# Kernel optimization log

Hardware: AMD Instinct MI355X
Metric: run time of the kernel (lower is better)

Reference implementation:

```python
import jax, jax.numpy as jnp
import numpy as np

D, NH, DH, DM = 1024, 16, 64, 4096
B, S = 2, 2048
EPS = 1e-5


def _layernorm(x, w, b):
    mu = jnp.mean(x, axis=-1, keepdims=True)
    var = jnp.mean((x - mu) ** 2, axis=-1, keepdims=True)
    return (x - mu) * jax.lax.rsqrt(var + EPS) * w + b


def setup_inputs() -> dict:
    key = jax.random.key(0)
    ks = jax.random.split(key, 8)
    scale = D ** (-0.5)
    x = jax.random.normal(ks[0], (B, S, D), dtype=jnp.float32)
    WQ = jax.random.normal(ks[1], (NH, D, DH), dtype=jnp.float32) * scale
    WK = jax.random.normal(ks[2], (NH, D, DH), dtype=jnp.float32) * scale
    WV = jax.random.normal(ks[3], (NH, D, DH), dtype=jnp.float32) * scale
    WO = jax.random.normal(ks[4], (NH, DH, D), dtype=jnp.float32) * scale
    # MLP: torch Linear default init ~ U(-1/sqrt(fan_in), 1/sqrt(fan_in)); stored as [in, out]
    W1 = jax.random.uniform(ks[5], (D, DM), dtype=jnp.float32, minval=-1.0, maxval=1.0) * D ** (-0.5)
    b1 = jnp.zeros((DM,), dtype=jnp.float32)
    W2 = jax.random.uniform(ks[6], (DM, D), dtype=jnp.float32, minval=-1.0, maxval=1.0) * DM ** (-0.5)
    b2 = jnp.zeros((D,), dtype=jnp.float32)
    ln1_w = jnp.ones((D,), dtype=jnp.float32)
    ln1_b = jnp.zeros((D,), dtype=jnp.float32)
    ln2_w = jnp.ones((D,), dtype=jnp.float32)
    ln2_b = jnp.zeros((D,), dtype=jnp.float32)
    return {"x": x, "WQ": WQ, "WK": WK, "WV": WV, "WO": WO,
            "W1": W1, "b1": b1, "W2": W2, "b2": b2,
            "ln1_w": ln1_w, "ln1_b": ln1_b, "ln2_w": ln2_w, "ln2_b": ln2_b}


def reference(x, WQ, WK, WV, WO, W1, b1, W2, b2, ln1_w, ln1_b, ln2_w, ln2_b):
    s = x.shape[1]
    dh = WQ.shape[-1]
    r = x
    h = _layernorm(x, ln1_w, ln1_b)
    # batched across all heads (original loops over h; math identical)
    Q = jnp.einsum('bsd,hde->bhse', h, WQ)
    K = jnp.einsum('bsd,hde->bhse', h, WK)
    V = jnp.einsum('bsd,hde->bhse', h, WV)
    scores = jnp.einsum('bhqe,bhke->bhqk', Q, K) / jnp.sqrt(jnp.float32(dh))
    causal = jnp.tril(jnp.ones((s, s), dtype=bool))  # True = keep
    scores = jnp.where(causal, scores, -jnp.inf)
    attn = jax.nn.softmax(scores, axis=-1)
    ctx = jnp.einsum('bhqk,bhke->bhqe', attn, V)
    ao = jnp.einsum('bhqe,hed->bqd', ctx, WO)  # sum over heads
    x = r + ao
    h2 = _layernorm(x, ln2_w, ln2_b)
    mlp = jax.nn.gelu(h2 @ W1 + b1, approximate=False) @ W2 + b2
    return x + mlp
```

## Files before the change

kernel.cpp:

```cpp
#include <hip/hip_runtime.h>
#include <hip/hip_bf16.h>
#include <cstdint>

#define D_MODEL 1024
#define NHEADS 16
#define DHEAD 64
#define DMLP 4096
#define BATCH 2
#define SEQ 2048
#define ROWS (BATCH*SEQ)
#define LN_EPS 1e-5f

typedef __attribute__((ext_vector_type(8))) short short8;
typedef __attribute__((ext_vector_type(4))) float f32x4;

typedef const __attribute__((address_space(1))) uint32_t* gas_ptr;
typedef __attribute__((address_space(3))) uint32_t* las_ptr;

__device__ __forceinline__ short f2bf(float f) {
  union { float f; uint32_t u; } v; v.f = f;
  uint32_t r = v.u + 0x7FFFu + ((v.u >> 16) & 1u);
  return (short)(r >> 16);
}
__device__ __forceinline__ float bf2f(short s) {
  union { uint32_t u; float f; } v; v.u = ((uint32_t)(uint16_t)s) << 16;
  return v.f;
}

__global__ void ln_kernel(const float* __restrict__ x, const float* __restrict__ w,
                          const float* __restrict__ b, short* __restrict__ out) {
  int row = blockIdx.x;
  int t = threadIdx.x;
  const float4 v = ((const float4*)(x + (size_t)row * D_MODEL))[t];
  float s = v.x + v.y + v.z + v.w;
  float s2 = v.x*v.x + v.y*v.y + v.z*v.z + v.w*v.w;
#pragma unroll
  for (int k = 1; k < 64; k <<= 1) { s += __shfl_xor(s, k); s2 += __shfl_xor(s2, k); }
  __shared__ float red[8];
  int wv = t >> 6;
  if ((t & 63) == 0) { red[wv] = s; red[wv + 4] = s2; }
  __syncthreads();
  s = red[0] + red[1] + red[2] + red[3];
  s2 = red[4] + red[5] + red[6] + red[7];
  float mu = s * (1.0f / D_MODEL);
  float var = s2 * (1.0f / D_MODEL) - mu * mu;
  float rstd = rsqrtf(var + LN_EPS);
  const float4 wv4 = ((const float4*)w)[t];
  const float4 bv4 = ((const float4*)b)[t];
  short4 o4;
  o4.x = f2bf((v.x - mu) * rstd * wv4.x + bv4.x);
  o4.y = f2bf((v.y - mu) * rstd * wv4.y + bv4.y);
  o4.z = f2bf((v.z - mu) * rstd * wv4.z + bv4.z);
  o4.w = f2bf((v.w - mu) * rstd * wv4.w + bv4.w);
  *(short4*)(out + (size_t)row * D_MODEL + t * 4) = o4;
}

__global__ void reduce_ln(float* __restrict__ out, const float* __restrict__ part,
                          const float* __restrict__ w, const float* __restrict__ b,
                          short* __restrict__ h2) {
  int row = blockIdx.x;
  int t = threadIdx.x;
  float4 v = ((float4*)(out + (size_t)row * D_MODEL))[t];
  const float4 q = ((const float4*)(part + (size_t)row * D_MODEL))[t];
  v.x += q.x; v.y += q.y; v.z += q.z; v.w += q.w;
  ((float4*)(out + (size_t)row * D_MODEL))[t] = v;
  float s = v.x + v.y + v.z + v.w;
  float s2 = v.x*v.x + v.y*v.y + v.z*v.z + v.w*v.w;
#pragma unroll
  for (int k = 1; k < 64; k <<= 1) { s += __shfl_xor(s, k); s2 += __shfl_xor(s2, k); }
  __shared__ float red[8];
  int wv = t >> 6;
  if ((t & 63) == 0) { red[wv] = s; red[wv + 4] = s2; }
  __syncthreads();
  s = red[0] + red[1] + red[2] + red[3];
  s2 = red[4] + red[5] + red[6] + red[7];
  float mu = s * (1.0f / D_MODEL);
  float var = s2 * (1.0f / D_MODEL) - mu * mu;
  float rstd = rsqrtf(var + LN_EPS);
  const float4 wv4 = ((const float4*)w)[t];
  const float4 bv4 = ((const float4*)b)[t];
  short4 o4;
  o4.x = f2bf((v.x - mu) * rstd * wv4.x + bv4.x);
  o4.y = f2bf((v.y - mu) * rstd * wv4.y + bv4.y);
  o4.z = f2bf((v.z - mu) * rstd * wv4.z + bv4.z);
  o4.w = f2bf((v.w - mu) * rstd * wv4.w + bv4.w);
  *(short4*)(h2 + (size_t)row * D_MODEL + t * 4) = o4;
}

__global__ __launch_bounds__(256) void repack_w(const float* __restrict__ W, short* __restrict__ out,
                                                int nkt, int ks1, int ks2, int ns1, int ns2) {
  const int cp = blockIdx.x, kt = blockIdx.y;
  const int t = threadIdx.x;
  const int cc = t & 127;
  const int kh = t >> 7;
  const int n = cp * 128 + cc;
  const int nbase = (n >> 6) * ns1 + (n & 63) * ns2;
  short* dst = out + (((size_t)cp * nkt + kt) * 128 + cc) * 64;
#pragma unroll
  for (int ci = 0; ci < 4; ci++) {
    const int c = kh * 4 + ci;
    short8 ch;
#pragma unroll
    for (int j = 0; j < 8; j++) {
      int k = kt * 64 + c * 8 + j;
      ch[j] = f2bf(W[(k >> 6) * ks1 + (k & 63) * ks2 + nbase]);
    }
    const int sp = c ^ (cc & 7);
    *(short8*)(dst + sp * 8) = ch;
  }
}

template<int EPI>
__global__ __launch_bounds__(256) void gemm_bt(const short* __restrict__ A, const short* __restrict__ Bpk,
    const float* __restrict__ bias, const float* __restrict__ resid,
    float* __restrict__ outf, short* __restrict__ outb, float* __restrict__ part,
    int M, int N, int K, int LDA, int KFULL) {
  __shared__ alignas(16) short As[2][8192];
  __shared__ alignas(16) short Bs[2][8192];
  const int t = threadIdx.x;
  const int l = t & 63, w = t >> 6;
  const int l15 = l & 15, l4 = l >> 4;

  const int nx = gridDim.x;
  const int sw = nx >> 3;
  int dd = blockIdx.y * nx + blockIdx.x;
  const int xcd = dd & 7, li = dd >> 3;
  const int bx = xcd * sw + (li % sw);
  const int by = li / sw;
  const int row0 = by * 128, col0 = bx * 128;

  const int NKT = KFULL >> 6;
  int ktB = 0;
  if (EPI == 5) {
    A  += (size_t)blockIdx.z * K;
    ktB = blockIdx.z * (K >> 6);
  }
  const short* Bpan = Bpk + (size_t)bx * NKT * 8192;

  f32x4 acc[4][4] = {};

  char* AsB = (char*)As;
  char* BsB = (char*)Bs;

  auto stg = [&](int ti) {
    const int bo = (ti & 1) * 16384;
    const int k0 = ti << 6;
    const short* bsrc = Bpan + (size_t)(ktB + ti) * 8192;
#pragma unroll
    for (int i = 0; i < 4; i++) {
      const int g = i * 256 + t;
      const int gr = g >> 3, sp = g & 7;
      const int co = k0 + ((sp ^ (gr & 7)) << 3);
      __builtin_amdgcn_global_load_lds((gas_ptr)(A + (size_t)(row0 + gr) * LDA + co),
                                       (las_ptr)(AsB + bo + g * 16), 16, 0, 0);
      __builtin_amdgcn_global_load_lds((gas_ptr)(bsrc + (size_t)g * 8),
                                       (las_ptr)(BsB + bo + g * 16), 16, 0, 0);
    }
  };

  const int nk = K >> 6;
  stg(0);
  asm volatile("s_waitcnt vmcnt(0)" ::: "memory");
  __builtin_amdgcn_s_barrier();

  const int wr = (w >> 1) * 64, wc = (w & 1) * 64;

  for (int ti = 0; ti < nk; ti++) {
    const int bo = (ti & 1) * 16384;
    if (ti + 1 < nk) stg(ti + 1);
#pragma unroll
    for (int kg = 0; kg < 2; kg++) {
      const int sl = ((kg * 4 + l4) ^ (l15 & 7)) * 16;
      short8 a[4], bfr[4];
#pragma unroll
      for (int m = 0; m < 4; m++) a[m]   = *(const short8*)(AsB + bo + (wr + m * 16 + l15) * 128 + sl);
#pragma unroll
      for (int n = 0; n < 4; n++) bfr[n] = *(const short8*)(BsB + bo + (wc + n * 16 + l15) * 128 + sl);
#pragma unroll
      for (int m = 0; m < 4; m++)
#pragma unroll
        for (int n = 0; n < 4; n++)
          acc[m][n] = __builtin_amdgcn_mfma_f32_16x16x32_bf16(a[m], bfr[n], acc[m][n], 0, 0, 0);
    }
    if (ti + 1 < nk) { asm volatile("s_waitcnt vmcnt(0)" ::: "memory"); }
    __builtin_amdgcn_s_barrier();
  }

#pragma unroll
  for (int m = 0; m < 4; m++) {
#pragma unroll
    for (int n = 0; n < 4; n++) {
#pragma unroll
      for (int j = 0; j < 4; j++) {
        int R_ = row0 + wr + m * 16 + l4 * 4 + j;
        int C_ = col0 + wc + n * 16 + l15;
        float v = acc[m][n][j];
        size_t o = (size_t)R_ * N + C_;
        if (EPI == 0) {
          outb[o] = f2bf(v);
        } else if (EPI == 2) {
          float xx = v + bias[C_];
          outb[o] = f2bf(0.5f * xx * (1.0f + erff(xx * 0.70710678118f)));
        } else if (EPI == 5) {
          if (blockIdx.z == 0) outf[o] = v + (bias ? bias[C_] : 0.0f) + resid[o];
          else part[o] = v;
        }
      }
    }
  }
}

__global__ void reduce1(float* __restrict__ out, const float* __restrict__ p, int n4) {
  for (int i = blockIdx.x * 256 + threadIdx.x; i < n4; i += gridDim.x * 256) {
    float4 o = ((float4*)out)[i];
    float4 q = ((const float4*)p)[i];
    o.x += q.x; o.y += q.y; o.z += q.z; o.w += q.w;
    ((float4*)out)[i] = o;
  }
}

__device__ __forceinline__ void attn_step(
    int kt_, int qt, int bufP,
    const short* __restrict__ base, const short* __restrict__ vbase,
    short8& vWA, short8& vWB,
    short8& vLA, short8& vLB,
    const short8 qf[2],
    char* KsB, char* VtB, char* PlB,
    f32x4 acc[4], float mrun[4], float lrun[4],
    int w, int l, int q0, int vr, int vd0)
{
  const int l15 = l & 15, l4 = l >> 4;
  const int bufQ = bufP ^ 1;
  if (kt_ < qt) {
#pragma unroll
    for (int i = 0; i < 8; i++) {
      int d = vd0 + i;
      int cs = (vr >> 2) ^ ((d >> 3) & 7);
      uint32_t val = (uint32_t)(uint16_t)vWA[i] | ((uint32_t)(uint16_t)vWB[i] << 16);
      *(uint32_t*)(VtB + bufQ * 9216 + d * 144 + cs * 16 + (vr & 3) * 4) = val;
    }
#pragma unroll
    for (int i = 0; i < 2; i++) {
      int g = (w * 2 + i) * 64 + l;
      int key = g >> 3, ck = g & 7;
      const short* src = base + (size_t)((kt_ + 1) * 64 + key) * 3072 + 1024 + ((ck ^ (key & 7)) * 8);
      __builtin_amdgcn_global_load_lds((gas_ptr)src, (las_ptr)(KsB + bufQ * 8192 + g * 16), 16, 0, 0);
    }
  }
  if (kt_ + 2 <= qt) {
    vLA = *(const short8*)(vbase + (size_t)((kt_ + 2) * 64 + 2 * vr) * 3072);
    vLB = *(const short8*)(vbase + (size_t)((kt_ + 2) * 64 + 2 * vr + 1) * 3072);
  }

  f32x4 sc[4];
#pragma unroll
  for (int cb = 0; cb < 4; cb++) {
    f32x4 s = {};
    int key = cb * 16 + l15;
#pragma unroll
    for (int c = 0; c < 2; c++) {
      int ck = (c * 4 + l4) ^ (key & 7);
      short8 kf = *(const short8*)(KsB + bufP * 8192 + key * 128 + ck * 16);
      s = __builtin_amdgcn_mfma_f32_16x16x32_bf16(qf[c], kf, s, 0, 0, 0);
    }
    sc[cb] = s;
  }

  const bool lastt = (kt_ == qt);
  float alpha[4];
#pragma unroll
  for (int jj = 0; jj < 4; jj++) {
    int qg = q0 + l4 * 4 + jj;
    float s0 = sc[0][jj] * 0.125f;
    float s1 = sc[1][jj] * 0.125f;
    float s2 = sc[2][jj] * 0.125f;
    float s3 = sc[3][jj] * 0.125f;
    if (lastt) {
      int kg = kt_ * 64 + l15;
      if (kg      > qg) s0 = -1e30f;
      if (kg + 16 > qg) s1 = -1e30f;
      if (kg + 32 > qg) s2 = -1e30f;
      if (kg + 48 > qg) s3 = -1e30f;
    }
    float rm = fmaxf(fmaxf(s0, s1), fmaxf(s2, s3));
    rm = fmaxf(rm, __shfl_xor(rm, 1));
    rm = fmaxf(rm, __shfl_xor(rm, 2));
    rm = fmaxf(rm, __shfl_xor(rm, 4));
    rm = fmaxf(rm, __shfl_xor(rm, 8));
    float nm = fmaxf(mrun[jj], rm);
    float al = __expf(mrun[jj] - nm);
    mrun[jj] = nm;
    float p0 = __expf(s0 - nm), p1 = __expf(s1 - nm);
    float p2 = __expf(s2 - nm), p3 = __expf(s3 - nm);
    float ps = p0 + p1 + p2 + p3;
    ps += __shfl_xor(ps, 1);
    ps += __shfl_xor(ps, 2);
    ps += __shfl_xor(ps, 4);
    ps += __shfl_xor(ps, 8);
    lrun[jj] = lrun[jj] * al + ps;
    alpha[jj] = al;
    short* pr = (short*)(PlB + (l4 * 4 + jj) * 144);
    pr[l15]      = f2bf(p0);
    pr[16 + l15] = f2bf(p1);
    pr[32 + l15] = f2bf(p2);
    pr[48 + l15] = f2bf(p3);
  }
#pragma unroll
  for (int db = 0; db < 4; db++) {
    f32x4 a = acc[db];
    a[0] *= alpha[0]; a[1] *= alpha[1]; a[2] *= alpha[2]; a[3] *= alpha[3];
    acc[db] = a;
  }
#pragma unroll
  for (int kc = 0; kc < 2; kc++) {
    short8 pf = *(const short8*)(PlB + l15 * 144 + kc * 64 + l4 * 16);
#pragma unroll
    for (int db = 0; db < 4; db++) {
      int d = db * 16 + l15;
      int cs = (kc * 4 + l4) ^ ((d >> 3) & 7);
      short8 vf = *(const short8*)(VtB + bufP * 9216 + d * 144 + cs * 16);
      acc[db] = __builtin_amdgcn_mfma_f32_16x16x32_bf16(pf, vf, acc[db], 0, 0, 0);
    }
  }
}

__global__ __launch_bounds__(256) void attn_mfma(const short* __restrict__ qkv, short* __restrict__ ctx) {
  __shared__ alignas(16) short Ks[2 * 64 * 64];
  __shared__ alignas(16) short Vt[2 * 64 * 72];
  __shared__ alignas(16) short Pl[4][16 * 72];
  const int t = threadIdx.x;
  const int l = t & 63;
  const int w = t >> 6;
  const int l15 = l & 15, l4 = l >> 4;
  const int bh = blockIdx.x;
  const int b = bh >> 4, h = bh & 15;
  const int qt = (gridDim.y - 1) - blockIdx.y;
  const int q0 = qt * 64 + w * 16;

  const short* base = qkv + (size_t)b * SEQ * 3072 + h * 64;

  short8 qf[2];
#pragma unroll
  for (int c = 0; c < 2; c++)
    qf[c] = *(const short8*)(base + (size_t)(q0 + l15) * 3072 + c * 32 + l4 * 8);

  const int vr = t >> 3;
  const int vd0 = (t & 7) * 8;
  const short* vbase = base + 2048 + vd0;

  char* KsB = (char*)Ks;
  char* VtB = (char*)Vt;
  char* PlB = (char*)&Pl[w][0];

  short8 va0, vb0, va1, vb1;
  va0 = *(const short8*)(vbase + (size_t)(2 * vr) * 3072);
  vb0 = *(const short8*)(vbase + (size_t)(2 * vr + 1) * 3072);
  if (qt >= 1) {
    va1 = *(const short8*)(vbase + (size_t)(64 + 2 * vr) * 3072);
    vb1 = *(const short8*)(vbase + (size_t)(64 + 2 * vr + 1) * 3072);
  }
#pragma unroll
  for (int i = 0; i < 8; i++) {
    int d = vd0 + i;
    int cs = (vr >> 2) ^ ((d >> 3) & 7);
    uint32_t val = (uint32_t)(uint16_t)va0[i] | ((uint32_t)(uint16_t)vb0[i] << 16);
    *(uint32_t*)(VtB + d * 144 + cs * 16 + (vr & 3) * 4) = val;
  }
#pragma unroll
  for (int i = 0; i < 2; i++) {
    int g = (w * 2 + i) * 64 + l;
    int key = g >> 3, ck = g & 7;
    const short* src = base + (size_t)key * 3072 + 1024 + ((ck ^ (key & 7)) * 8);
    __builtin_amdgcn_global_load_lds((gas_ptr)src, (las_ptr)(KsB + g * 16), 16, 0, 0);
  }
  __syncthreads();

  f32x4 acc[4] = {};
  float mrun[4] = {-1e30f, -1e30f, -1e30f, -1e30f};
  float lrun[4] = {0.f, 0.f, 0.f, 0.f};

  int kt = 0;
  while (true) {
    attn_step(kt, qt, 0, base, vbase, va1, vb1, va0, vb0, qf,
              KsB, VtB, PlB, acc, mrun, lrun, w, l, q0, vr, vd0);
    __syncthreads();
    if (++kt > qt) break;
    attn_step(kt, qt, 1, base, vbase, va0, vb0, va1, vb1, qf,
              KsB, VtB, PlB, acc, mrun, lrun, w, l, q0, vr, vd0);
    __syncthreads();
    if (++kt > qt) break;
  }

  float inv[4];
#pragma unroll
  for (int jj = 0; jj < 4; jj++) inv[jj] = 1.0f / lrun[jj];
  short* obase = ctx + (size_t)(b * SEQ + q0) * D_MODEL + h * 64;
#pragma unroll
  for (int db = 0; db < 4; db++)
#pragma unroll
    for (int jj = 0; jj < 4; jj++)
      obase[(size_t)(l4 * 4 + jj) * D_MODEL + db * 16 + l15] = f2bf(acc[db][jj] * inv[jj]);
}

extern "C" void kernel_launch(void* const* d_in, const int* in_sizes, int n_in,
                              void* d_out, int out_size, void* d_ws, size_t ws_size,
                              hipStream_t stream) {
  (void)in_sizes; (void)n_in; (void)out_size; (void)ws_size;
  const float* x    = (const float*)d_in[0];
  const float* WQ   = (const float*)d_in[1];
  const float* WK   = (const float*)d_in[2];
  const float* WV   = (const float*)d_in[3];
  const float* WO   = (const float*)d_in[4];
  const float* W1   = (const float*)d_in[5];
  const float* b1   = (const float*)d_in[6];
  const float* W2   = (const float*)d_in[7];
  const float* b2   = (const float*)d_in[8];
  const float* ln1w = (const float*)d_in[9];
  const float* ln1b = (const float*)d_in[10];
  const float* ln2w = (const float*)d_in[11];
  const float* ln2b = (const float*)d_in[12];
  float* out = (float*)d_out;

  char* p = (char*)d_ws;
  short* h1    = (short*)p; p += (size_t)ROWS * D_MODEL * 2;
  short* ctx   = (short*)p; p += (size_t)ROWS * D_MODEL * 2;
  short* h2    = (short*)p; p += (size_t)ROWS * D_MODEL * 2;
  short* m1    = (short*)p; p += (size_t)ROWS * DMLP * 2;
  short* wqkvT = (short*)p; p += (size_t)3 * D_MODEL * D_MODEL * 2;
  short* woT   = (short*)p; p += (size_t)D_MODEL * D_MODEL * 2;
  short* w1T   = (short*)p; p += (size_t)D_MODEL * DMLP * 2;
  short* w2T   = (short*)p; p += (size_t)D_MODEL * DMLP * 2;
  short* qkv   = (short*)p; p += (size_t)ROWS * 3 * D_MODEL * 2;

  float* fp1 = (float*)qkv;

  repack_w<<<dim3(8, 16), 256, 0, stream>>>(WQ, wqkvT,                 16, 4096, 64, 65536, 1);
  repack_w<<<dim3(8, 16), 256, 0, stream>>>(WK, wqkvT + 8 * 16 * 8192, 16, 4096, 64, 65536, 1);
  repack_w<<<dim3(8, 16), 256, 0, stream>>>(WV, wqkvT + 16 * 16 * 8192, 16, 4096, 64, 65536, 1);
  repack_w<<<dim3(8, 16), 256, 0, stream>>>(WO, woT, 16, 65536, 1024, 64, 1);
  repack_w<<<dim3(32, 16), 256, 0, stream>>>(W1, w1T, 16, 262144, 4096, 64, 1);
  repack_w<<<dim3(8, 64), 256, 0, stream>>>(W2, w2T, 64, 65536, 1024, 64, 1);

  ln_kernel<<<ROWS, 256, 0, stream>>>(x, ln1w, ln1b, h1);
  gemm_bt<0><<<dim3(3 * D_MODEL / 128, ROWS / 128), 256, 0, stream>>>(
      h1, wqkvT, nullptr, nullptr, nullptr, qkv, nullptr,
      ROWS, 3 * D_MODEL, D_MODEL, D_MODEL, D_MODEL);
  attn_mfma<<<dim3(BATCH * NHEADS, SEQ / 64), 256, 0, stream>>>(qkv, ctx);
  gemm_bt<5><<<dim3(D_MODEL / 128, ROWS / 128, 2), 256, 0, stream>>>(
      ctx, woT, nullptr, x, out, nullptr, fp1,
      ROWS, D_MODEL, D_MODEL / 2, D_MODEL, D_MODEL);
  reduce_ln<<<ROWS, 256, 0, stream>>>(out, fp1, ln2w, ln2b, h2);
  gemm_bt<2><<<dim3(DMLP / 128, ROWS / 128), 256, 0, stream>>>(
      h2, w1T, b1, nullptr, nullptr, m1, nullptr,
      ROWS, DMLP, D_MODEL, D_MODEL, D_MODEL);
  gemm_bt<5><<<dim3(D_MODEL / 128, ROWS / 128, 2), 256, 0, stream>>>(
      m1, w2T, b2, out, out, nullptr, fp1,
      ROWS, D_MODEL, DMLP / 2, DMLP, DMLP);
  reduce1<<<2048, 256, 0, stream>>>(out, fp1, ROWS * D_MODEL / 4);
}
```

Baseline: 299.9 us.

## Double attention query tile per block and precompute GEMM staging pointers

The attention kernel now gives each block 128 queries, with each wave handling 32 rows, so every K/V tile loaded into LDS is reused by twice as many queries. The grid halves and uses an interleaved long/short tile order for load balance. Causal masking is applied whenever a key tile overlaps the wave's query range. The GEMM staging loop also precomputes its global and LDS addresses and advances them incrementally instead of recomputing swizzled offsets each tile. The cost is higher register pressure and fewer blocks for the attention kernel.

```diff
diff --git a/kernel.cpp b/kernel.cpp
--- a/kernel.cpp
+++ b/kernel.cpp
@@ -135,31 +135,36 @@
     A  += (size_t)blockIdx.z * K;
     ktB = blockIdx.z * (K >> 6);
   }
-  const short* Bpan = Bpk + (size_t)bx * NKT * 8192;
 
   f32x4 acc[4][4] = {};
-
   char* AsB = (char*)As;
   char* BsB = (char*)Bs;
 
-  auto stg = [&](int ti) {
-    const int bo = (ti & 1) * 16384;
-    const int k0 = ti << 6;
-    const short* bsrc = Bpan + (size_t)(ktB + ti) * 8192;
+  const short* aP[4];
+#pragma unroll
+  for (int i = 0; i < 4; i++) {
+    const int g = i * 256 + t;
+    const int gr = g >> 3, sp = g & 7;
+    aP[i] = A + (size_t)(row0 + gr) * LDA + ((sp ^ (gr & 7)) << 3);
+  }
+  const short* bP = Bpk + ((size_t)bx * NKT + ktB) * 8192 + t * 8;
+  const int d16 = t * 16;
+  int sb = 0;
+
+  auto stg = [&]() {
 #pragma unroll
     for (int i = 0; i < 4; i++) {
-      const int g = i * 256 + t;
-      const int gr = g >> 3, sp = g & 7;
-      const int co = k0 + ((sp ^ (gr & 7)) << 3);
-      __builtin_amdgcn_global_load_lds((gas_ptr)(A + (size_t)(row0 + gr) * LDA + co),
-                                       (las_ptr)(AsB + bo + g * 16), 16, 0, 0);
-      __builtin_amdgcn_global_load_lds((gas_ptr)(bsrc + (size_t)g * 8),
-                                       (las_ptr)(BsB + bo + g * 16), 16, 0, 0);
-    }
+      __builtin_amdgcn_global_load_lds((gas_ptr)(aP[i]),          (las_ptr)(AsB + sb + i * 4096 + d16), 16, 0, 0);
+      __builtin_amdgcn_global_load_lds((gas_ptr)(bP + i * 2048),  (las_ptr)(BsB + sb + i * 4096 + d16), 16, 0, 0);
+    }
+#pragma unroll
+    for (int i = 0; i < 4; i++) aP[i] += 64;
+    bP += 8192;
+    sb ^= 16384;
   };
 
   const int nk = K >> 6;
-  stg(0);
+  stg();
   asm volatile("s_waitcnt vmcnt(0)" ::: "memory");
   __builtin_amdgcn_s_barrier();
 
@@ -167,7 +172,7 @@
 
   for (int ti = 0; ti < nk; ti++) {
     const int bo = (ti & 1) * 16384;
-    if (ti + 1 < nk) stg(ti + 1);
+    if (ti + 1 < nk) stg();
 #pragma unroll
     for (int kg = 0; kg < 2; kg++) {
       const int sl = ((kg * 4 + l4) ^ (l15 & 7)) * 16;
@@ -220,18 +225,18 @@
 }
 
 __device__ __forceinline__ void attn_step(
-    int kt_, int qt, int bufP,
+    int kt_, int ntm1, int bufP,
     const short* __restrict__ base, const short* __restrict__ vbase,
     short8& vWA, short8& vWB,
     short8& vLA, short8& vLB,
-    const short8 qf[2],
+    const short8 qf[2][2],
     char* KsB, char* VtB, char* PlB,
-    f32x4 acc[4], float mrun[4], float lrun[4],
-    int w, int l, int q0, int vr, int vd0)
+    f32x4 acc[2][4], float mrun[2][4], float lrun[2][4],
+    int w, int l, int q0w, int vr, int vd0)
 {
   const int l15 = l & 15, l4 = l >> 4;
   const int bufQ = bufP ^ 1;
-  if (kt_ < qt) {
+  if (kt_ < ntm1) {
 #pragma unroll
     for (int i = 0; i < 8; i++) {
       int d = vd0 + i;
@@ -247,79 +252,87 @@
       __builtin_amdgcn_global_load_lds((gas_ptr)src, (las_ptr)(KsB + bufQ * 8192 + g * 16), 16, 0, 0);
     }
   }
-  if (kt_ + 2 <= qt) {
+  if (kt_ + 2 <= ntm1) {
     vLA = *(const short8*)(vbase + (size_t)((kt_ + 2) * 64 + 2 * vr) * 3072);
     vLB = *(const short8*)(vbase + (size_t)((kt_ + 2) * 64 + 2 * vr + 1) * 3072);
   }
 
-  f32x4 sc[4];
+  f32x4 sc[2][4];
 #pragma unroll
   for (int cb = 0; cb < 4; cb++) {
-    f32x4 s = {};
+    f32x4 s0 = {}, s1 = {};
     int key = cb * 16 + l15;
 #pragma unroll
     for (int c = 0; c < 2; c++) {
       int ck = (c * 4 + l4) ^ (key & 7);
       short8 kf = *(const short8*)(KsB + bufP * 8192 + key * 128 + ck * 16);
-      s = __builtin_amdgcn_mfma_f32_16x16x32_bf16(qf[c], kf, s, 0, 0, 0);
-    }
-    sc[cb] = s;
-  }
-
-  const bool lastt = (kt_ == qt);
-  float alpha[4];
-#pragma unroll
-  for (int jj = 0; jj < 4; jj++) {
-    int qg = q0 + l4 * 4 + jj;
-    float s0 = sc[0][jj] * 0.125f;
-    float s1 = sc[1][jj] * 0.125f;
-    float s2 = sc[2][jj] * 0.125f;
-    float s3 = sc[3][jj] * 0.125f;
-    if (lastt) {
-      int kg = kt_ * 64 + l15;
-      if (kg      > qg) s0 = -1e30f;
-      if (kg + 16 > qg) s1 = -1e30f;
-      if (kg + 32 > qg) s2 = -1e30f;
-      if (kg + 48 > qg) s3 = -1e30f;
-    }
-    float rm = fmaxf(fmaxf(s0, s1), fmaxf(s2, s3));
-    rm = fmaxf(rm, __shfl_xor(rm, 1));
-    rm = fmaxf(rm, __shfl_xor(rm, 2));
-    rm = fmaxf(rm, __shfl_xor(rm, 4));
-    rm = fmaxf(rm, __shfl_xor(rm, 8));
-    float nm = fmaxf(mrun[jj], rm);
-    float al = __expf(mrun[jj] - nm);
-    mrun[jj] = nm;
-    float p0 = __expf(s0 - nm), p1 = __expf(s1 - nm);
-    float p2 = __expf(s2 - nm), p3 = __expf(s3 - nm);
-    float ps = p0 + p1 + p2 + p3;
-    ps += __shfl_xor(ps, 1);
-    ps += __shfl_xor(ps, 2);
-    ps += __shfl_xor(ps, 4);
-    ps += __shfl_xor(ps, 8);
-    lrun[jj] = lrun[jj] * al + ps;
-    alpha[jj] = al;
-    short* pr = (short*)(PlB + (l4 * 4 + jj) * 144);
-    pr[l15]      = f2bf(p0);
-    pr[16 + l15] = f2bf(p1);
-    pr[32 + l15] = f2bf(p2);
-    pr[48 + l15] = f2bf(p3);
-  }
-#pragma unroll
-  for (int db = 0; db < 4; db++) {
-    f32x4 a = acc[db];
-    a[0] *= alpha[0]; a[1] *= alpha[1]; a[2] *= alpha[2]; a[3] *= alpha[3];
-    acc[db] = a;
-  }
+      s0 = __builtin_amdgcn_mfma_f32_16x16x32_bf16(qf[0][c], kf, s0, 0, 0, 0);
+      s1 = __builtin_amdgcn_mfma_f32_16x16x32_bf16(qf[1][c], kf, s1, 0, 0, 0);
+    }
+    sc[0][cb] = s0; sc[1][cb] = s1;
+  }
+
+  const bool needm = (kt_ * 64 + 63 > q0w);
+  float alpha[2][4];
+#pragma unroll
+  for (int r = 0; r < 2; r++) {
+#pragma unroll
+    for (int jj = 0; jj < 4; jj++) {
+      int qg = q0w + r * 16 + l4 * 4 + jj;
+      float s0 = sc[r][0][jj] * 0.125f;
+      float s1 = sc[r][1][jj] * 0.125f;
+      float s2 = sc[r][2][jj] * 0.125f;
+      float s3 = sc[r][3][jj] * 0.125f;
+      if (needm) {
+        int kg = kt_ * 64 + l15;
+        if (kg      > qg) s0 = -1e30f;
+        if (kg + 16 > qg) s1 = -1e30f;
+        if (kg + 32 > qg) s2 = -1e30f;
+        if (kg + 48 > qg) s3 = -1e30f;
+      }
+      float rm = fmaxf(fmaxf(s0, s1), fmaxf(s2, s3));
+      rm = fmaxf(rm, __shfl_xor(rm, 1));
+      rm = fmaxf(rm, __shfl_xor(rm, 2));
+      rm = fmaxf(rm, __shfl_xor(rm, 4));
+      rm = fmaxf(rm, __shfl_xor(rm, 8));
+      float nm = fmaxf(mrun[r][jj], rm);
+      float al = __expf(mrun[r][jj] - nm);
+      mrun[r][jj] = nm;
+      float p0 = __expf(s0 - nm), p1 = __expf(s1 - nm);
+      float p2 = __expf(s2 - nm), p3 = __expf(s3 - nm);
+      float ps = p0 + p1 + p2 + p3;
+      ps += __shfl_xor(ps, 1);
+      ps += __shfl_xor(ps, 2);
+      ps += __shfl_xor(ps, 4);
+      ps += __shfl_xor(ps, 8);
+      lrun[r][jj] = lrun[r][jj] * al + ps;
+      alpha[r][jj] = al;
+      short* pr = (short*)(PlB + (r * 16 + l4 * 4 + jj) * 144);
+      pr[l15]      = f2bf(p0);
+      pr[16 + l15] = f2bf(p1);
+      pr[32 + l15] = f2bf(p2);
+      pr[48 + l15] = f2bf(p3);
+    }
+  }
+#pragma unroll
+  for (int r = 0; r < 2; r++)
+#pragma unroll
+    for (int db = 0; db < 4; db++) {
+      f32x4 a = acc[r][db];
+      a[0] *= alpha[r][0]; a[1] *= alpha[r][1]; a[2] *= alpha[r][2]; a[3] *= alpha[r][3];
+      acc[r][db] = a;
+    }
 #pragma unroll
   for (int kc = 0; kc < 2; kc++) {
-    short8 pf = *(const short8*)(PlB + l15 * 144 + kc * 64 + l4 * 16);
+    short8 pf0 = *(const short8*)(PlB + l15 * 144 + kc * 64 + l4 * 16);
+    short8 pf1 = *(const short8*)(PlB + (16 + l15) * 144 + kc * 64 + l4 * 16);
 #pragma unroll
     for (int db = 0; db < 4; db++) {
       int d = db * 16 + l15;
       int cs = (kc * 4 + l4) ^ ((d >> 3) & 7);
       short8 vf = *(const short8*)(VtB + bufP * 9216 + d * 144 + cs * 16);
-      acc[db] = __builtin_amdgcn_mfma_f32_16x16x32_bf16(pf, vf, acc[db], 0, 0, 0);
+      acc[0][db] = __builtin_amdgcn_mfma_f32_16x16x32_bf16(pf0, vf, acc[0][db], 0, 0, 0);
+      acc[1][db] = __builtin_amdgcn_mfma_f32_16x16x32_bf16(pf1, vf, acc[1][db], 0, 0, 0);
     }
   }
 }
@@ -327,22 +340,26 @@
 __global__ __launch_bounds__(256) void attn_mfma(const short* __restrict__ qkv, short* __restrict__ ctx) {
   __shared__ alignas(16) short Ks[2 * 64 * 64];
   __shared__ alignas(16) short Vt[2 * 64 * 72];
-  __shared__ alignas(16) short Pl[4][16 * 72];
+  __shared__ alignas(16) short Pl[4][32 * 72];
   const int t = threadIdx.x;
   const int l = t & 63;
   const int w = t >> 6;
   const int l15 = l & 15, l4 = l >> 4;
   const int bh = blockIdx.x;
   const int b = bh >> 4, h = bh & 15;
-  const int qt = (gridDim.y - 1) - blockIdx.y;
-  const int q0 = qt * 64 + w * 16;
+  const int y = blockIdx.y;
+  const int qt = (y < 8) ? (15 - 2 * y) : (2 * (y - 8));
+  const int q0w = qt * 128 + w * 32;
+  const int ntm1 = 2 * qt + 1;
 
   const short* base = qkv + (size_t)b * SEQ * 3072 + h * 64;
 
-  short8 qf[2];
-#pragma unroll
-  for (int c = 0; c < 2; c++)
-    qf[c] = *(const short8*)(base + (size_t)(q0 + l15) * 3072 + c * 32 + l4 * 8);
+  short8 qf[2][2];
+#pragma unroll
+  for (int r = 0; r < 2; r++)
+#pragma unroll
+    for (int c = 0; c < 2; c++)
+      qf[r][c] = *(const short8*)(base + (size_t)(q0w + r * 16 + l15) * 3072 + c * 32 + l4 * 8);
 
   const int vr = t >> 3;
   const int vd0 = (t & 7) * 8;
@@ -355,10 +372,8 @@
   short8 va0, vb0, va1, vb1;
   va0 = *(const short8*)(vbase + (size_t)(2 * vr) * 3072);
   vb0 = *(const short8*)(vbase + (size_t)(2 * vr + 1) * 3072);
-  if (qt >= 1) {
-    va1 = *(const short8*)(vbase + (size_t)(64 + 2 * vr) * 3072);
-    vb1 = *(const short8*)(vbase + (size_t)(64 + 2 * vr + 1) * 3072);
-  }
+  va1 = *(const short8*)(vbase + (size_t)(64 + 2 * vr) * 3072);
+  vb1 = *(const short8*)(vbase + (size_t)(64 + 2 * vr + 1) * 3072);
 #pragma unroll
   for (int i = 0; i < 8; i++) {
     int d = vd0 + i;
@@ -375,31 +390,33 @@
   }
   __syncthreads();
 
-  f32x4 acc[4] = {};
-  float mrun[4] = {-1e30f, -1e30f, -1e30f, -1e30f};
-  float lrun[4] = {0.f, 0.f, 0.f, 0.f};
+  f32x4 acc[2][4] = {};
+  float mrun[2][4] = {{-1e30f, -1e30f, -1e30f, -1e30f}, {-1e30f, -1e30f, -1e30f, -1e30f}};
+  float lrun[2][4] = {{0.f, 0.f, 0.f, 0.f}, {0.f, 0.f, 0.f, 0.f}};
 
   int kt = 0;
   while (true) {
-    attn_step(kt, qt, 0, base, vbase, va1, vb1, va0, vb0, qf,
-              KsB, VtB, PlB, acc, mrun, lrun, w, l, q0, vr, vd0);
+    attn_step(kt, ntm1, 0, base, vbase, va1, vb1, va0, vb0, qf,
+              KsB, VtB, PlB, acc, mrun, lrun, w, l, q0w, vr, vd0);
     __syncthreads();
-    if (++kt > qt) break;
-    attn_step(kt, qt, 1, base, vbase, va0, vb0, va1, vb1, qf,
-              KsB, VtB, PlB, acc, mrun, lrun, w, l, q0, vr, vd0);
+    if (++kt > ntm1) break;
+    attn_step(kt, ntm1, 1, base, vbase, va0, vb0, va1, vb1, qf,
+              KsB, VtB, PlB, acc, mrun, lrun, w, l, q0w, vr, vd0);
     __syncthreads();
-    if (++kt > qt) break;
-  }
-
-  float inv[4];
-#pragma unroll
-  for (int jj = 0; jj < 4; jj++) inv[jj] = 1.0f / lrun[jj];
-  short* obase = ctx + (size_t)(b * SEQ + q0) * D_MODEL + h * 64;
-#pragma unroll
-  for (int db = 0; db < 4; db++)
-#pragma unroll
-    for (int jj = 0; jj < 4; jj++)
-      obase[(size_t)(l4 * 4 + jj) * D_MODEL + db * 16 + l15] = f2bf(acc[db][jj] * inv[jj]);
+    if (++kt > ntm1) break;
+  }
+
+  short* obase = ctx + (size_t)(b * SEQ + q0w) * D_MODEL + h * 64;
+#pragma unroll
+  for (int r = 0; r < 2; r++) {
+#pragma unroll
+    for (int jj = 0; jj < 4; jj++) {
+      float inv = 1.0f / lrun[r][jj];
+#pragma unroll
+      for (int db = 0; db < 4; db++)
+        obase[(size_t)(r * 16 + l4 * 4 + jj) * D_MODEL + db * 16 + l15] = f2bf(acc[r][db][jj] * inv);
+    }
+  }
 }
 
 extern "C" void kernel_launch(void* const* d_in, const int* in_sizes, int n_in,
@@ -434,8 +451,8 @@
 
   float* fp1 = (float*)qkv;
 
-  repack_w<<<dim3(8, 16), 256, 0, stream>>>(WQ, wqkvT,                 16, 4096, 64, 65536, 1);
-  repack_w<<<dim3(8, 16), 256, 0, stream>>>(WK, wqkvT + 8 * 16 * 8192, 16, 4096, 64, 65536, 1);
+  repack_w<<<dim3(8, 16), 256, 0, stream>>>(WQ, wqkvT,                  16, 4096, 64, 65536, 1);
+  repack_w<<<dim3(8, 16), 256, 0, stream>>>(WK, wqkvT + 8 * 16 * 8192,  16, 4096, 64, 65536, 1);
   repack_w<<<dim3(8, 16), 256, 0, stream>>>(WV, wqkvT + 16 * 16 * 8192, 16, 4096, 64, 65536, 1);
   repack_w<<<dim3(8, 16), 256, 0, stream>>>(WO, woT, 16, 65536, 1024, 64, 1);
   repack_w<<<dim3(32, 16), 256, 0, stream>>>(W1, w1T, 16, 262144, 4096, 64, 1);
@@ -445,7 +462,7 @@
   gemm_bt<0><<<dim3(3 * D_MODEL / 128, ROWS / 128), 256, 0, stream>>>(
       h1, wqkvT, nullptr, nullptr, nullptr, qkv, nullptr,
       ROWS, 3 * D_MODEL, D_MODEL, D_MODEL, D_MODEL);
-  attn_mfma<<<dim3(BATCH * NHEADS, SEQ / 64), 256, 0, stream>>>(qkv, ctx);
+  attn_mfma<<<dim3(BATCH * NHEADS, SEQ / 128), 256, 0, stream>>>(qkv, ctx);
   gemm_bt<5><<<dim3(D_MODEL / 128, ROWS / 128, 2), 256, 0, stream>>>(
       ctx, woT, nullptr, x, out, nullptr, fp1,
       ROWS, D_MODEL, D_MODEL / 2, D_MODEL, D_MODEL);
```

After: 402.3 us. 1.34x slower.
